# Optimization experiments

Hardware: AMD Instinct MI355X
Metric: run time of the kernel (lower is better)

## Reference

```python
import jax, jax.numpy as jnp
import numpy as np

B, S, D, H = 64, 65536, 512, 256
H2 = H // 2
CAP_LIMIT = 0.85
ACT_THR = 0.5


def _normalize(x):
    return x / jnp.maximum(jnp.linalg.norm(x, axis=-1, keepdims=True), 1e-12)


def _layernorm(x, g, b):
    m = x.mean(-1, keepdims=True)
    v = ((x - m) ** 2).mean(-1, keepdims=True)
    return (x - m) / jnp.sqrt(v + 1e-5) * g + b


def setup_inputs() -> dict:
    key = jax.random.key(0)
    ks = jax.random.split(key, 20)

    def lin(k, i, o):
        s = 1.0 / np.sqrt(i)
        kw, kb = jax.random.split(k)
        return (jax.random.uniform(kw, (i, o), minval=-s, maxval=s),
                jax.random.uniform(kb, (o,), minval=-s, maxval=s))

    inp = {}
    inp["new_content"] = jax.random.normal(ks[0], (B, D), dtype=jnp.float32)
    inp["query"] = jax.random.normal(ks[1], (B, D), dtype=jnp.float32)
    inp["memory_bank"] = jax.random.normal(ks[2], (S, D), dtype=jnp.float32)
    inp["access_times"] = jax.random.uniform(ks[3], (S,), minval=0.0, maxval=900.0)
    inp["current_step"] = 1000
    inp["sr_w1"], inp["sr_b1"] = lin(ks[4], 2 * D, H)
    inp["sr_g"] = jnp.ones((H,), jnp.float32)
    inp["sr_beta"] = jnp.zeros((H,), jnp.float32)
    inp["sr_w2"], inp["sr_b2"] = lin(ks[5], H, H2)
    inp["sn_w"], inp["sn_b"] = lin(ks[6], D, H2)
    inp["sg_w"], inp["sg_b"] = lin(ks[7], H2, 1)
    inp["el_w"], inp["el_b"] = lin(ks[8], 1, 32)
    inp["ec_w"], inp["ec_b"] = lin(ks[9], D, 32)
    inp["eg_w"], inp["eg_b"] = lin(ks[10], 64, 1)
    inp["dd_w1"], inp["dd_b1"] = lin(ks[11], 2 * D, H)
    inp["dd_w2"], inp["dd_b2"] = lin(ks[12], H, 1)
    inp["ds_w1"], inp["ds_b1"] = lin(ks[13], 2 * D, H)
    inp["ds_w2"], inp["ds_b2"] = lin(ks[14], H, 1)
    return inp


def _forward(new_content, query, memory_bank, access_times,
             sr_w1, sr_b1, sr_g, sr_beta, sr_w2, sr_b2,
             sn_w, sn_b, sg_w, sg_b,
             el_w, el_b, ec_w, ec_b, eg_w, eg_b,
             dd_w1, dd_b1, dd_w2, dd_b2,
             ds_w1, ds_b1, ds_w2, ds_b2,
             step):
    mem = memory_bank
    at = access_times
    norms = jnp.linalg.norm(mem, axis=-1)               # [S]
    capacity = jnp.mean((norms > ACT_THR).astype(jnp.float32))
    dyn_thr = jnp.clip(
        jnp.where(capacity < 0.3, 0.08,
                  jnp.where(capacity < 0.6, 0.08 + (capacity - 0.3) * 0.733,
                            0.3 + (capacity - 0.6))), 0.0, 0.7)
    topk_thr = jnp.where(capacity < 0.3, 0.1, jnp.where(capacity < 0.6, 0.2, 0.4))
    raw_thr = jnp.where(capacity < 0.3, 0.3, 0.5)

    # store relevance / novelty / gate
    combined = jnp.concatenate([new_content, query], -1)          # [B,2D]
    h = _layernorm(combined @ sr_w1 + sr_b1, sr_g, sr_beta)
    rel = jax.nn.relu(jax.nn.relu(h) @ sr_w2 + sr_b2)             # [B,H2]
    nn_ = _normalize(new_content)
    sims = nn_ @ _normalize(mem).T                                # [B,S]
    max_sim = sims.max(-1, keepdims=True)
    novelty = (1.0 - max_sim) / 2.0                               # [B,1]
    nf = jax.nn.sigmoid(new_content @ sn_w + sn_b)
    store_score = jax.nn.sigmoid((rel + nf) @ sg_w + sg_b)        # [B,1]

    # novelty percentile over active slots (no boolean-shape gather)
    active = norms > ACT_THR
    n_active = active.sum()
    nov_mean = novelty.mean()
    cond = (nov_mean > (1.0 - sims)) & active[None, :]
    denom = (new_content.shape[0] * jnp.maximum(n_active, 1)).astype(jnp.float32)
    perc = jnp.where(n_active > 0, cond.sum().astype(jnp.float32) / denom, 1.0)

    base_store = store_score.mean() > raw_thr
    novelty_ok = nov_mean > dyn_thr
    topk_ok = perc > topk_thr
    should_store = base_store & novelty_ok & topk_ok

    # emergency erase (capacity over limit)
    do_erase = capacity > CAP_LIMIT
    age = jnp.maximum(step - at, 0.0)
    es_em = age / (age.max() + 1e-6) + (1.0 - jax.nn.sigmoid(norms))
    victim = jnp.argmax(es_em)
    mem = jnp.where(do_erase, mem.at[victim].set(0.0), mem)
    at = jnp.where(do_erase, at.at[victim].set(-99999.0), at)
    should_store = should_store & jnp.logical_not(do_erase & jnp.logical_not(novelty_ok))

    # per-slot erase scores
    lru = jax.nn.relu(((step - at) / 1000.0)[:, None] @ el_w + el_b)   # [S,32]
    conf = jax.nn.sigmoid(mem @ ec_w + ec_b)                            # [S,32]
    erase_scores = jax.nn.sigmoid(jnp.concatenate([lru, conf], -1) @ eg_w + eg_b)[:, 0]

    # conflict detection: top-3 similar slots, gather-MLP-scatter drift
    sims2 = _normalize(new_content) @ _normalize(mem).T                # [B,S]
    tv, ti = jax.lax.top_k(sims2, 3)                                   # [B,3]
    cmask = (tv > 0.7) & (tv < 0.99)
    gathered = mem[ti]                                                 # [B,3,D]
    pair = jnp.concatenate([jnp.broadcast_to(new_content[:, None, :], gathered.shape), gathered], -1)
    prob = jax.nn.sigmoid(jax.nn.relu(pair @ dd_w1 + dd_b1) @ dd_w2 + dd_b2)[..., 0]
    strength = jax.nn.sigmoid(jax.nn.relu(pair @ ds_w1 + ds_b1) @ ds_w2 + ds_b2)[..., 0]
    apply_m = cmask & (prob > 0.5)                                     # [B,3]
    avg = (new_content[:, None, :] + gathered) / 2.0
    s = strength[..., None]
    dn_cand = (1.0 - s) * new_content[:, None, :] + s * avg
    do_cand = (1.0 - s) * gathered + s * avg
    drifted_new = new_content
    for k in range(3):  # fixed k=3, later k overwrites (matches torch inner loop)
        drifted_new = jnp.where(apply_m[:, k:k + 1], dn_cand[:, k], drifted_new)
    for k in range(3):
        idx = ti[:, k]
        cur = mem[idx]
        mem = mem.at[idx].set(jnp.where(apply_m[:, k, None], do_cand[:, k], cur))

    # conditional write
    slot_age = step - at
    recent = (at >= 0.0) & (slot_age < 3.0)
    masked = erase_scores * (~recent).astype(erase_scores.dtype)
    masked = jnp.where(masked.max() <= 0.0, slot_age, masked)
    write_idx = jnp.where(do_erase, victim, jnp.argmax(masked))
    erase_out = jnp.where(should_store & jnp.logical_not(do_erase), masked, erase_scores)
    mem = jnp.where(should_store, mem.at[write_idx].set(drifted_new[0]), mem)
    at = jnp.where(should_store, at.at[write_idx].set(step), at)

    recent_changes = jnp.abs(mem - memory_bank).mean()
    return (mem, at, erase_out, store_score[:, 0], novelty[:, 0], recent_changes)


def reference(new_content, query, memory_bank, access_times,
              sr_w1, sr_b1, sr_g, sr_beta, sr_w2, sr_b2,
              sn_w, sn_b, sg_w, sg_b,
              el_w, el_b, ec_w, ec_b, eg_w, eg_b,
              dd_w1, dd_b1, dd_w2, dd_b2,
              ds_w1, ds_b1, ds_w2, ds_b2,
              current_step):
    step = jnp.float32(current_step)
    return _forward(new_content, query, memory_bank, access_times,
                    sr_w1, sr_b1, sr_g, sr_beta, sr_w2, sr_b2,
                    sn_w, sn_b, sg_w, sg_b,
                    el_w, el_b, ec_w, ec_b, eg_w, eg_b,
                    dd_w1, dd_b1, dd_w2, dd_b2,
                    ds_w1, ds_b1, ds_w2, ds_b2, step)
```

## Files before the change

### kernel.cpp

```cpp
#include <hip/hip_runtime.h>
#include <math.h>
#include <limits.h>

#define S_N 65536
#define D_N 512
#define B_N 64

typedef __attribute__((ext_vector_type(8))) short short8;
typedef __attribute__((ext_vector_type(4))) float f32x4;

#define SIMS_F      (B_N*S_N/2)
#define OFF_SIMS    0
#define OFF_AEXT    (OFF_SIMS + SIMS_F)
#define AEXT_F      (96*512/2)
#define OFF_NORMS   (OFF_AEXT + AEXT_F)
#define OFF_CONF    (OFF_NORMS + S_N)
#define OFF_FLAGS   (OFF_CONF + S_N)
#define OFF_LIST    (OFF_FLAGS + S_N)
#define OFF_MASKED  (OFF_LIST + 256)
#define OFF_ERSC    (OFF_MASKED + S_N)
#define OFF_SLOTAGE (OFF_ERSC + S_N)
#define OFF_STORES  (OFF_SLOTAGE + S_N)
#define OFF_MAXSIM  (OFF_STORES + 64)
#define OFF_TI      (OFF_MAXSIM + 64)
#define OFF_TV      (OFF_TI + 192)
#define OFF_APPLY   (OFF_TV + 192)
#define OFF_HM      (OFF_APPLY + 192)
#define OFF_HNC     (OFF_HM + 32768)
#define OFF_HG      (OFF_HNC + 65536)
#define OFF_DNC0    (OFF_HG + 196608)
#define OFF_DRIFT0  (OFF_DNC0 + 1536)
#define OFF_DOCAND  (OFF_DRIFT0 + 512)
#define OFF_SCAL    (OFF_DOCAND + 98304)

#define OUT_MEM 0
#define OUT_AT  (S_N*D_N)
#define OUT_ER  (OUT_AT + S_N)
#define OUT_SS  (OUT_ER + S_N)
#define OUT_NOV (OUT_SS + 64)
#define OUT_RC  (OUT_NOV + 64)

struct __align__(8) Scal {
  unsigned long long victim_pack;
  unsigned long long masked_pack;
  unsigned long long slotage_pack;
  int cnt_active;
  int cond_cnt;
  unsigned age_max_t;
  float nov_mean;
  float changed_sum;
  int do_erase;
  int should_store;
  int write_idx;
  int victim_idx;
  int list_cnt;
};

__device__ __forceinline__ float sigmoidf_(float x){ return 1.0f/(1.0f+expf(-x)); }
__device__ __forceinline__ unsigned f2mono(float f){
  unsigned u = __float_as_uint(f);
  return (u & 0x80000000u) ? ~u : (u | 0x80000000u);
}
__device__ __forceinline__ float mono2f(unsigned m){
  unsigned u = (m & 0x80000000u) ? (m & 0x7FFFFFFFu) : ~m;
  return __uint_as_float(u);
}
__device__ __forceinline__ unsigned long long packvi(float v, int i){
  return (((unsigned long long)f2mono(v)) << 32) | (unsigned long long)(0xFFFFFFFFu - (unsigned)i);
}
__device__ __forceinline__ bool betterVI(float v, int i, float v2, int i2){
  return (v > v2) || (v == v2 && i < i2);
}
__device__ __forceinline__ unsigned short bf16r(float f){
  unsigned u = __float_as_uint(f);
  return (unsigned short)((u + 0x7fffu + ((u>>16)&1u)) >> 16);
}
__device__ __forceinline__ float bf2f(unsigned short h){
  return __uint_as_float(((unsigned)h)<<16);
}
__device__ __forceinline__ void touch_row(int row, float* ws){
  int* flags = (int*)(ws + OFF_FLAGS);
  if (atomicExch(&flags[row], 1) == 0){
    Scal* sc = (Scal*)(ws + OFF_SCAL);
    int i = atomicAdd(&sc->list_cnt, 1);
    ((int*)(ws + OFF_LIST))[i] = row;
  }
}

__global__ __launch_bounds__(256) void k_init(const float* __restrict__ nc,
                                              const float* __restrict__ at_in,
                                              const float* __restrict__ ec_w,
                                              const int* __restrict__ step_p,
                                              float* __restrict__ ws, float* __restrict__ out){
  int blk = blockIdx.x, t = threadIdx.x;
  Scal* sc = (Scal*)(ws + OFF_SCAL);
  unsigned short* aB = (unsigned short*)(ws + OFF_AEXT);
  if (blk == 0){
    if (t == 0){
      sc->victim_pack = 0ULL; sc->masked_pack = 0ULL; sc->slotage_pack = 0ULL;
      sc->cnt_active = 0; sc->cond_cnt = 0; sc->age_max_t = 0u;
      sc->nov_mean = 0.0f; sc->changed_sum = 0.0f;
      sc->do_erase = 0; sc->should_store = 0; sc->write_idx = 0; sc->victim_idx = 0;
      sc->list_cnt = 0;
    }
    if (t < 64) ((unsigned*)(ws + OFF_MAXSIM))[t] = 0u;
  } else if (blk <= 64){
    int b = blk - 1;
    __shared__ float red[256];
    float x0 = nc[b*512 + t], x1 = nc[b*512 + 256 + t];
    red[t] = x0*x0 + x1*x1;
    __syncthreads();
    for (int o=128;o>0;o>>=1){ if (t<o) red[t]+=red[t+o]; __syncthreads(); }
    float inv = 1.0f / fmaxf(sqrtf(red[0]), 1e-12f);
    aB[b*512 + t]       = bf16r(x0*inv);
    aB[b*512 + 256 + t] = bf16r(x1*inv);
  } else if (blk <= 96){
    int j = blk - 65;
    for (int d=t; d<512; d+=256) aB[(64+j)*512 + d] = bf16r(ec_w[d*32 + j]);
  } else if (blk <= 160){
    int part = blk - 97;
    float stepf = (float)step_p[0];
    float lmax = -1e30f;
    for (int s = part*1024 + t; s < (part+1)*1024; s += 256)
      lmax = fmaxf(lmax, fmaxf(stepf - at_in[s], 0.0f));
    __shared__ float red[256];
    red[t]=lmax; __syncthreads();
    for (int o=128;o>0;o>>=1){ if (t<o) red[t]=fmaxf(red[t],red[t+o]); __syncthreads(); }
    if (t==0) atomicMax(&sc->age_max_t, f2mono(red[0]));
  } else if (blk <= 224){
    int part = blk - 161;
    for (int s = part*1024 + t; s < (part+1)*1024; s += 256)
      out[OUT_AT + s] = at_in[s];
  } else {
    int part = blk - 225;
    int* flags = (int*)(ws + OFF_FLAGS);
    for (int s = part*1024 + t; s < (part+1)*1024; s += 256) flags[s] = 0;
  }
}

#define BT_ST 520
__global__ __launch_bounds__(256,2) void k_phase1(const float* __restrict__ mem,
                                                  const float* __restrict__ ec_b,
                                                  const float* __restrict__ eg_w,
                                                  float* __restrict__ ws, float* __restrict__ out){
  __shared__ unsigned short lB[64*BT_ST];
  __shared__ float nred[256];
  __shared__ float linv[64];
  __shared__ unsigned lmax[64];
  int t = threadIdx.x;
  int s0 = blockIdx.x * 64;
  if (t < 64) lmax[t] = 0u;
  Scal* sc = (Scal*)(ws + OFF_SCAL);

  const float4* mem4 = (const float4*)(mem + (size_t)s0*512);
  float4* out4 = (float4*)(out + OUT_MEM + (size_t)s0*512);
  #pragma unroll
  for (int i=0;i<32;i++){
    int idx = i*256 + t;
    float4 v = mem4[idx];
    out4[idx] = v;
    int row = idx >> 7, c4 = idx & 127;
    unsigned u0 = (((unsigned)bf16r(v.y))<<16) | bf16r(v.x);
    unsigned u1 = (((unsigned)bf16r(v.w))<<16) | bf16r(v.z);
    uint2* dst = (uint2*)&lB[row*BT_ST + c4*4];
    *dst = make_uint2(u0,u1);
  }
  __syncthreads();

  {
    int row = t>>2, q = t&3;
    const unsigned* src = (const unsigned*)&lB[row*BT_ST + q*128];
    float ssq = 0.f;
    #pragma unroll
    for (int i=0;i<64;i++){
      unsigned u = src[i];
      float a = __uint_as_float(u<<16);
      float b = __uint_as_float(u & 0xffff0000u);
      ssq = fmaf(a,a,ssq); ssq = fmaf(b,b,ssq);
    }
    nred[t] = ssq;
  }
  __syncthreads();
  if (t < 64){
    float s2 = nred[t*4]+nred[t*4+1]+nred[t*4+2]+nred[t*4+3];
    float nrm = sqrtf(s2);
    ws[OFF_NORMS + s0 + t] = nrm;
    linv[t] = 1.0f / fmaxf(nrm, 1e-12f);
    unsigned long long m = __ballot(nrm > 0.5f);
    if (t == 0) atomicAdd(&sc->cnt_active, (int)__popcll(m));
  }
  __syncthreads();

  int lane = t & 63, wv = t >> 6;
  int quad = lane >> 4, l15 = lane & 15;
  const unsigned short* aB = (const unsigned short*)(ws + OFF_AEXT);
  f32x4 acc[6];
  #pragma unroll
  for (int r=0;r<6;r++) acc[r] = (f32x4){0.f,0.f,0.f,0.f};
  #pragma unroll 4
  for (int kc=0;kc<16;kc++){
    int kb = kc*32 + quad*8;
    short8 bfrag = *(const short8*)&lB[(wv*16 + l15)*BT_ST + kb];
    #pragma unroll
    for (int rt=0;rt<6;rt++){
      short8 afrag = *(const short8*)&aB[(rt*16 + l15)*512 + kb];
      acc[rt] = __builtin_amdgcn_mfma_f32_16x16x32_bf16(afrag, bfrag, acc[rt], 0,0,0);
    }
  }

  float lv = linv[wv*16 + l15];
  unsigned short* simsb = (unsigned short*)(ws + OFF_SIMS);
  #pragma unroll
  for (int rt=0;rt<4;rt++){
    #pragma unroll
    for (int r=0;r<4;r++){
      int a = rt*16 + quad*4 + r;
      float sim = acc[rt][r] * lv;
      simsb[(size_t)a*S_N + s0 + wv*16 + l15] = bf16r(sim);
      atomicMax(&lmax[a], f2mono(sim));
    }
  }
  float cpart = 0.f;
  #pragma unroll
  for (int rt=4;rt<6;rt++){
    #pragma unroll
    for (int r=0;r<4;r++){
      int j = (rt-4)*16 + quad*4 + r;
      cpart += sigmoidf_(acc[rt][r] + ec_b[j]) * eg_w[32+j];
    }
  }
  cpart += __shfl_down(cpart, 32);
  cpart += __shfl_down(cpart, 16);
  if (l15 < 16 && quad == 0) ws[OFF_CONF + s0 + wv*16 + l15] = cpart;
  __syncthreads();
  if (t < 64) atomicMax(((unsigned*)(ws + OFF_MAXSIM)) + t, lmax[t]);
}

__global__ __launch_bounds__(256) void k_mlp1a(const float* __restrict__ nc, const float* __restrict__ qr,
    const float* __restrict__ sr_w1, float* __restrict__ ws){
  int blk = blockIdx.x, t = threadIdx.x;
  int b = blk >> 1, half = blk & 1;
  __shared__ float ch[512];
  const float* src = half ? qr : nc;
  ch[t] = src[b*512 + t]; ch[256+t] = src[b*512 + 256 + t];
  __syncthreads();
  float h = 0.f;
  const float* w = sr_w1 + (half*512)*256 + t;
  for (int i=0;i<512;i++) h = fmaf(ch[i], w[i*256], h);
  ws[OFF_HM + (half*64 + b)*256 + t] = h;
}

__global__ __launch_bounds__(256) void k_mlp1b(const float* __restrict__ nc, const float* __restrict__ qr,
    const float* __restrict__ sr_b1, const float* __restrict__ sr_g, const float* __restrict__ sr_beta,
    const float* __restrict__ sr_w2, const float* __restrict__ sr_b2,
    const float* __restrict__ sn_w,  const float* __restrict__ sn_b,
    const float* __restrict__ sg_w,  const float* __restrict__ sg_b,
    float* __restrict__ ws, float* __restrict__ out){
  int b = blockIdx.x, t = threadIdx.x;
  Scal* sc = (Scal*)(ws + OFF_SCAL);
  __shared__ float red[256];
  if (b == 64){
    const unsigned* gms = (const unsigned*)(ws + OFF_MAXSIM);
    float nv = 0.0f;
    if (t < 64){
      float msim = mono2f(gms[t]);
      nv = (1.0f - msim) * 0.5f;
      out[OUT_NOV + t] = nv;
    }
    red[t] = (t < 64) ? nv : 0.0f;
    __syncthreads();
    for (int o=128;o>0;o>>=1){ if (t<o) red[t]+=red[t+o]; __syncthreads(); }
    if (t == 0) sc->nov_mean = red[0] / 64.0f;
    return;
  }
  __shared__ float comb[1024];
  __shared__ float hbuf[256];
  comb[t]       = nc[b*512 + t];
  comb[256 + t] = nc[b*512 + 256 + t];
  comb[512 + t] = qr[b*512 + t];
  comb[768 + t] = qr[b*512 + 256 + t];
  float h = ws[OFF_HM + b*256 + t] + ws[OFF_HM + (64 + b)*256 + t] + sr_b1[t];
  red[t] = h; __syncthreads();
  for (int o=128;o>0;o>>=1){ if (t<o) red[t]+=red[t+o]; __syncthreads(); }
  float mean = red[0] / 256.0f;
  __syncthreads();
  float dx = h - mean;
  red[t] = dx*dx; __syncthreads();
  for (int o=128;o>0;o>>=1){ if (t<o) red[t]+=red[t+o]; __syncthreads(); }
  float var = red[0] / 256.0f;
  __syncthreads();
  float hn = dx / sqrtf(var + 1e-5f) * sr_g[t] + sr_beta[t];
  hbuf[t] = fmaxf(hn, 0.0f);
  __syncthreads();
  float val = 0.0f;
  if (t < 128){
    float r = sr_b2[t];
    for (int j=0;j<256;j++) r = fmaf(hbuf[j], sr_w2[j*128 + t], r);
    r = fmaxf(r, 0.0f);
    float nf = sn_b[t];
    for (int d=0; d<512; d++) nf = fmaf(comb[d], sn_w[d*128 + t], nf);
    nf = sigmoidf_(nf);
    val = (r + nf) * sg_w[t];
  }
  red[t] = val; __syncthreads();
  for (int o=128;o>0;o>>=1){ if (t<o) red[t]+=red[t+o]; __syncthreads(); }
  if (t == 0){
    float ssc = sigmoidf_(red[0] + sg_b[0]);
    out[OUT_SS + b] = ssc;
    ws[OFF_STORES + b] = ssc;
  }
}

__global__ __launch_bounds__(256) void k_scan(const float* __restrict__ at_in,
                                              const int* __restrict__ step_p,
                                              float* __restrict__ ws){
  int t = threadIdx.x;
  Scal* sc = (Scal*)(ws + OFF_SCAL);
  float thr = 1.0f - sc->nov_mean;
  float stepf = (float)step_p[0];
  float agemax = mono2f(sc->age_max_t);
  const unsigned* simsu = (const unsigned*)(ws + OFF_SIMS);
  const float* norms = ws + OFF_NORMS;
  int gid = blockIdx.x*256 + t;
  int gstride = gridDim.x*256;
  int cnt = 0;
  for (int idx = gid; idx < B_N*S_N/2; idx += gstride){
    unsigned u = simsu[idx];
    int s = (idx*2) & (S_N-1);
    float v0 = __uint_as_float(u<<16);
    float v1 = __uint_as_float(u & 0xffff0000u);
    if (v0 > thr && norms[s]   > 0.5f) cnt++;
    if (v1 > thr && norms[s+1] > 0.5f) cnt++;
  }
  unsigned long long best = 0ULL;
  for (int s = gid; s < S_N; s += gstride){
    float age = fmaxf(stepf - at_in[s], 0.0f);
    float es = age/(agemax + 1e-6f) + (1.0f - sigmoidf_(norms[s]));
    unsigned long long pk = packvi(es, s);
    if (pk > best) best = pk;
  }
  __shared__ int redc[256];
  __shared__ unsigned long long redp[256];
  redc[t] = cnt; redp[t] = best;
  __syncthreads();
  for (int o=128;o>0;o>>=1){
    if (t<o){ redc[t]+=redc[t+o]; if (redp[t+o] > redp[t]) redp[t]=redp[t+o]; }
    __syncthreads();
  }
  if (t == 0){
    atomicAdd(&sc->cond_cnt, redc[0]);
    atomicMax(&sc->victim_pack, redp[0]);
  }
}

__global__ __launch_bounds__(256) void k_victimfix(const float* __restrict__ ec_b,
                                                   const float* __restrict__ eg_w,
                                                   float* __restrict__ ws, float* __restrict__ out){
  int t = threadIdx.x;
  Scal* sc = (Scal*)(ws + OFF_SCAL);
  float capacity = (float)sc->cnt_active / 65536.0f;
  int de = (capacity > 0.85f) ? 1 : 0;
  int victim = (int)(0xFFFFFFFFu - (unsigned)(sc->victim_pack & 0xFFFFFFFFULL));
  if (t == 0){ sc->do_erase = de; sc->victim_idx = victim; }
  if (de){
    for (int d=t; d<512; d+=256) out[OUT_MEM + victim*512 + d] = 0.0f;
    if (t == 0){
      out[OUT_AT + victim] = -99999.0f;
      touch_row(victim, ws);
      float sum = 0.0f;
      for (int j=0;j<32;j++) sum += sigmoidf_(ec_b[j]) * eg_w[32 + j];
      ws[OFF_CONF + victim] = sum;
    }
  }
}

__global__ __launch_bounds__(256) void k_top3(float* __restrict__ ws){
  int b = blockIdx.x, t = threadIdx.x;
  Scal* sc = (Scal*)(ws + OFF_SCAL);
  int de = sc->do_erase;
  int victim = sc->victim_idx;
  const unsigned short* simrow = (const unsigned short*)(ws + OFF_SIMS) + (size_t)b*S_N;
  float v[3] = {-1e30f,-1e30f,-1e30f};
  int ix[3] = {INT_MAX, INT_MAX, INT_MAX};
  for (int s = t; s < S_N; s += 256){
    float val = bf2f(simrow[s]);
    if (de && s == victim) val = 0.0f;
    if (betterVI(val, s, v[2], ix[2])){
      if (betterVI(val, s, v[1], ix[1])){
        if (betterVI(val, s, v[0], ix[0])){
          v[2]=v[1]; ix[2]=ix[1]; v[1]=v[0]; ix[1]=ix[0]; v[0]=val; ix[0]=s;
        } else { v[2]=v[1]; ix[2]=ix[1]; v[1]=val; ix[1]=s; }
      } else { v[2]=val; ix[2]=s; }
    }
  }
  __shared__ float sv[256*3];
  __shared__ int   si[256*3];
  for (int r=0;r<3;r++){ sv[t*3+r]=v[r]; si[t*3+r]=ix[r]; }
  for (int off=128; off>0; off>>=1){
    __syncthreads();
    if (t < off){
      float av[3], bv[3], ov[3]; int ai[3], bi[3], oi[3];
      for (int r=0;r<3;r++){ av[r]=sv[t*3+r]; ai[r]=si[t*3+r]; bv[r]=sv[(t+off)*3+r]; bi[r]=si[(t+off)*3+r]; }
      int ap=0, bp=0;
      for (int r=0;r<3;r++){
        bool takeA = (bp>=3) || (ap<3 && betterVI(av[ap],ai[ap],bv[bp],bi[bp]));
        if (takeA){ ov[r]=av[ap]; oi[r]=ai[ap]; ap++; }
        else      { ov[r]=bv[bp]; oi[r]=bi[bp]; bp++; }
      }
      for (int r=0;r<3;r++){ sv[t*3+r]=ov[r]; si[t*3+r]=oi[r]; }
    }
  }
  __syncthreads();
  if (t == 0){
    for (int k=0;k<3;k++){
      ws[OFF_TV + b*3 + k] = sv[k];
      ((int*)(ws + OFF_TI))[b*3 + k] = si[k];
    }
  }
}

__global__ __launch_bounds__(256) void k_mlp2(const float* __restrict__ nc,
    const float* __restrict__ dd_w1, const float* __restrict__ ds_w1,
    float* __restrict__ ws, float* __restrict__ out){
  int blk = blockIdx.x, t = threadIdx.x;
  int b = blk >> 2, ks = blk & 3;
  __shared__ float ch[3*256];
  if (ks < 2){
    ch[t] = nc[b*512 + ks*256 + t];
    __syncthreads();
    float hd = 0.f, hs = 0.f;
    const float* wd = dd_w1 + (ks*256)*256 + t;
    const float* wq = ds_w1 + (ks*256)*256 + t;
    for (int i=0;i<256;i++){
      float c = ch[i];
      hd = fmaf(c, wd[i*256], hd);
      hs = fmaf(c, wq[i*256], hs);
    }
    float* H = ws + OFF_HNC + ((ks*64 + b)*2)*256;
    H[t] = hd; H[256 + t] = hs;
  } else {
    int ks2 = ks - 2;
    const int* tip = (const int*)(ws + OFF_TI);
    int r0 = tip[b*3], r1 = tip[b*3+1], r2 = tip[b*3+2];
    ch[t]       = out[OUT_MEM + (size_t)r0*512 + ks2*256 + t];
    ch[256 + t] = out[OUT_MEM + (size_t)r1*512 + ks2*256 + t];
    ch[512 + t] = out[OUT_MEM + (size_t)r2*512 + ks2*256 + t];
    __syncthreads();
    float hd0=0,hd1=0,hd2=0,hs0=0,hs1=0,hs2=0;
    const float* wd = dd_w1 + (512 + ks2*256)*256 + t;
    const float* wq = ds_w1 + (512 + ks2*256)*256 + t;
    for (int i=0;i<256;i++){
      float w0 = wd[i*256], w1 = wq[i*256];
      float c0 = ch[i], c1 = ch[256+i], c2 = ch[512+i];
      hd0=fmaf(c0,w0,hd0); hd1=fmaf(c1,w0,hd1); hd2=fmaf(c2,w0,hd2);
      hs0=fmaf(c0,w1,hs0); hs1=fmaf(c1,w1,hs1); hs2=fmaf(c2,w1,hs2);
    }
    float* H = ws + OFF_HG;
    int p0 = b*3;
    H[((ks2*192 + p0+0)*2+0)*256 + t] = hd0;
    H[((ks2*192 + p0+1)*2+0)*256 + t] = hd1;
    H[((ks2*192 + p0+2)*2+0)*256 + t] = hd2;
    H[((ks2*192 + p0+0)*2+1)*256 + t] = hs0;
    H[((ks2*192 + p0+1)*2+1)*256 + t] = hs1;
    H[((ks2*192 + p0+2)*2+1)*256 + t] = hs2;
  }
}

__global__ __launch_bounds__(256) void k_pairfin(const float* __restrict__ nc,
    const float* __restrict__ dd_b1, const float* __restrict__ dd_w2, const float* __restrict__ dd_b2,
    const float* __restrict__ ds_b1, const float* __restrict__ ds_w2, const float* __restrict__ ds_b2,
    float* __restrict__ ws, float* __restrict__ out){
  int p = blockIdx.x, t = threadIdx.x;
  int b = p / 3, k = p - 3*b;
  const int* tip = (const int*)(ws + OFF_TI);
  int row = tip[p];
  float hd = ws[OFF_HNC + ((0*64+b)*2+0)*256 + t] + ws[OFF_HNC + ((1*64+b)*2+0)*256 + t]
           + ws[OFF_HG + ((0*192+p)*2+0)*256 + t] + ws[OFF_HG + ((1*192+p)*2+0)*256 + t] + dd_b1[t];
  float hs = ws[OFF_HNC + ((0*64+b)*2+1)*256 + t] + ws[OFF_HNC + ((1*64+b)*2+1)*256 + t]
           + ws[OFF_HG + ((0*192+p)*2+1)*256 + t] + ws[OFF_HG + ((1*192+p)*2+1)*256 + t] + ds_b1[t];
  __shared__ float red[256];
  __shared__ float bc[2];
  red[t] = fmaxf(hd, 0.f) * dd_w2[t];
  __syncthreads();
  for (int o=128;o>0;o>>=1){ if (t<o) red[t]+=red[t+o]; __syncthreads(); }
  if (t == 0) bc[0] = red[0] + dd_b2[0];
  __syncthreads();
  red[t] = fmaxf(hs, 0.f) * ds_w2[t];
  __syncthreads();
  for (int o=128;o>0;o>>=1){ if (t<o) red[t]+=red[t+o]; __syncthreads(); }
  if (t == 0) bc[1] = red[0] + ds_b2[0];
  __syncthreads();
  float prob  = sigmoidf_(bc[0]);
  float stren = sigmoidf_(bc[1]);
  float tvv = ws[OFF_TV + p];
  int ap = (tvv > 0.7f && tvv < 0.99f && prob > 0.5f) ? 1 : 0;
  if (t == 0){
    ((int*)(ws + OFF_APPLY))[p] = ap;
    touch_row(row, ws);
  }
  for (int d=t; d<512; d+=256){
    float n = nc[b*512 + d];
    float g = out[OUT_MEM + (size_t)row*512 + d];
    float avg = 0.5f*(n + g);
    ws[OFF_DOCAND + p*512 + d] = (1.0f - stren)*g + stren*avg;
    if (b == 0) ws[OFF_DNC0 + k*512 + d] = (1.0f - stren)*n + stren*avg;
  }
}

__global__ __launch_bounds__(64) void k_scatter(float* __restrict__ ws, float* __restrict__ out){
  int d = blockIdx.x*64 + threadIdx.x;
  const int* tip = (const int*)(ws + OFF_TI);
  const int* ap  = (const int*)(ws + OFF_APPLY);
  for (int k=0;k<3;k++){
    float cur[64];
    #pragma unroll
    for (int b=0;b<64;b++) cur[b] = out[OUT_MEM + (size_t)tip[b*3 + k]*512 + d];
    #pragma unroll
    for (int b=0;b<64;b++){
      int p = b*3 + k;
      float v = ap[p] ? ws[OFF_DOCAND + p*512 + d] : cur[b];
      out[OUT_MEM + (size_t)tip[p]*512 + d] = v;
    }
  }
}

__global__ __launch_bounds__(256) void k_erase(const int* __restrict__ step_p,
    const float* __restrict__ el_w, const float* __restrict__ el_b,
    const float* __restrict__ eg_w, const float* __restrict__ eg_b,
    float* __restrict__ ws, float* __restrict__ out){
  int t = threadIdx.x;
  Scal* sc = (Scal*)(ws + OFF_SCAL);
  float stepf = (float)step_p[0];
  float egb = eg_b[0];
  int gid = blockIdx.x*256 + t;
  int gstride = gridDim.x*256;
  unsigned long long bm = 0ULL, bs = 0ULL;
  for (int s = gid; s < S_N; s += gstride){
    float a = out[OUT_AT + s];
    float x = (stepf - a) / 1000.0f;
    float lp = 0.0f;
    #pragma unroll
    for (int j=0;j<32;j++) lp += fmaxf(x*el_w[j] + el_b[j], 0.0f) * eg_w[j];
    float er = sigmoidf_(lp + ws[OFF_CONF + s] + egb);
    float sa = stepf - a;
    bool recent = (a >= 0.0f) && (sa < 3.0f);
    float msk = recent ? 0.0f : er;
    ws[OFF_ERSC + s] = er;
    ws[OFF_MASKED + s] = msk;
    ws[OFF_SLOTAGE + s] = sa;
    unsigned long long pm = packvi(msk, s); if (pm > bm) bm = pm;
    unsigned long long ps = packvi(sa,  s); if (ps > bs) bs = ps;
  }
  __shared__ unsigned long long rm[256], rs[256];
  rm[t]=bm; rs[t]=bs; __syncthreads();
  for (int o=128;o>0;o>>=1){
    if (t<o){ if (rm[t+o]>rm[t]) rm[t]=rm[t+o]; if (rs[t+o]>rs[t]) rs[t]=rs[t+o]; }
    __syncthreads();
  }
  if (t == 0){
    atomicMax(&sc->masked_pack, rm[0]);
    atomicMax(&sc->slotage_pack, rs[0]);
  }
}

__global__ __launch_bounds__(64) void k_decide(const float* __restrict__ nc, float* __restrict__ ws){
  int t = threadIdx.x;
  Scal* sc = (Scal*)(ws + OFF_SCAL);
  __shared__ float red[64];
  red[t] = ws[OFF_STORES + t];
  __syncthreads();
  for (int o=32;o>0;o>>=1){ if (t<o) red[t]+=red[t+o]; __syncthreads(); }
  if (t == 0){
    float store_mean = red[0] / 64.0f;
    int cnt = sc->cnt_active;
    float capacity = (float)cnt / 65536.0f;
    float dyn_thr;
    if (capacity < 0.3f) dyn_thr = 0.08f;
    else if (capacity < 0.6f) dyn_thr = 0.08f + (capacity - 0.3f)*0.733f;
    else dyn_thr = 0.3f + (capacity - 0.6f);
    dyn_thr = fminf(fmaxf(dyn_thr, 0.0f), 0.7f);
    float topk_thr = (capacity < 0.3f) ? 0.1f : ((capacity < 0.6f) ? 0.2f : 0.4f);
    float raw_thr  = (capacity < 0.3f) ? 0.3f : 0.5f;
    int base_store = store_mean > raw_thr;
    int novelty_ok = sc->nov_mean > dyn_thr;
    int cmax = cnt > 1 ? cnt : 1;
    float denom = (float)(64 * cmax);
    float perc = (cnt > 0) ? ((float)sc->cond_cnt) / denom : 1.0f;
    int topk_ok = perc > topk_thr;
    int de = sc->do_erase;
    int ss = base_store && novelty_ok && topk_ok;
    if (de && !novelty_ok) ss = 0;
    float mmax = mono2f((unsigned)(sc->masked_pack >> 32));
    int marg = (int)(0xFFFFFFFFu - (unsigned)(sc->masked_pack  & 0xFFFFFFFFULL));
    int sarg = (int)(0xFFFFFFFFu - (unsigned)(sc->slotage_pack & 0xFFFFFFFFULL));
    sc->should_store = ss;
    sc->write_idx = de ? sc->victim_idx : ((mmax > 0.0f) ? marg : sarg);
  }
  __syncthreads();
  const int* ap = (const int*)(ws + OFF_APPLY);
  for (int d=t; d<512; d+=64){
    float v = nc[d];
    if (ap[0]) v = ws[OFF_DNC0 + 0*512 + d];
    if (ap[1]) v = ws[OFF_DNC0 + 1*512 + d];
    if (ap[2]) v = ws[OFF_DNC0 + 2*512 + d];
    ws[OFF_DRIFT0 + d] = v;
  }
}

__global__ __launch_bounds__(256) void k_finalout(const int* __restrict__ step_p,
                                                  float* __restrict__ ws, float* __restrict__ out){
  int blk = blockIdx.x, t = threadIdx.x;
  Scal* sc = (Scal*)(ws + OFF_SCAL);
  int ss = sc->should_store, de = sc->do_erase;
  if (blk == 64){
    if (ss){
      int wi = sc->write_idx;
      for (int d=t; d<512; d+=256) out[OUT_MEM + (size_t)wi*512 + d] = ws[OFF_DRIFT0 + d];
      if (t == 0){
        out[OUT_AT + wi] = (float)step_p[0];
        touch_row(wi, ws);
      }
    }
    return;
  }
  float mmax = mono2f((unsigned)(sc->masked_pack >> 32));
  bool usemask = ss && !de;
  for (int s = blk*256 + t; s < S_N; s += 64*256){
    float v;
    if (usemask) v = (mmax <= 0.0f) ? ws[OFF_SLOTAGE + s] : ws[OFF_MASKED + s];
    else v = ws[OFF_ERSC + s];
    out[OUT_ER + s] = v;
  }
}

__global__ __launch_bounds__(256) void k_diff(const float* __restrict__ mem,
                                              float* __restrict__ ws, float* __restrict__ out){
  int t = threadIdx.x;
  Scal* sc = (Scal*)(ws + OFF_SCAL);
  int cnt = sc->list_cnt;
  const int* list = (const int*)(ws + OFF_LIST);
  float lsum = 0.0f;
  for (int i = blockIdx.x; i < cnt; i += gridDim.x){
    int row = list[i];
    float part = 0.0f;
    for (int d=t; d<512; d+=256)
      part += fabsf(out[OUT_MEM + (size_t)row*512 + d] - mem[(size_t)row*512 + d]);
    lsum += part;
  }
  __shared__ float red[256];
  red[t] = lsum; __syncthreads();
  for (int o=128;o>0;o>>=1){ if (t<o) red[t]+=red[t+o]; __syncthreads(); }
  if (t == 0 && red[0] != 0.0f) atomicAdd(&sc->changed_sum, red[0]);
}

__global__ void k_rc(float* __restrict__ ws, float* __restrict__ out){
  if (threadIdx.x == 0 && blockIdx.x == 0){
    Scal* sc = (Scal*)(ws + OFF_SCAL);
    out[OUT_RC] = sc->changed_sum / 33554432.0f;
  }
}

extern "C" void kernel_launch(void* const* d_in, const int* in_sizes, int n_in,
                              void* d_out, int out_size, void* d_ws, size_t ws_size,
                              hipStream_t stream) {
  const float* nc    = (const float*)d_in[0];
  const float* qr    = (const float*)d_in[1];
  const float* mem   = (const float*)d_in[2];
  const float* at    = (const float*)d_in[3];
  const int*   step  = (const int*)  d_in[4];
  const float* sr_w1 = (const float*)d_in[5];
  const float* sr_b1 = (const float*)d_in[6];
  const float* sr_g  = (const float*)d_in[7];
  const float* sr_be = (const float*)d_in[8];
  const float* sr_w2 = (const float*)d_in[9];
  const float* sr_b2 = (const float*)d_in[10];
  const float* sn_w  = (const float*)d_in[11];
  const float* sn_b  = (const float*)d_in[12];
  const float* sg_w  = (const float*)d_in[13];
  const float* sg_b  = (const float*)d_in[14];
  const float* el_w  = (const float*)d_in[15];
  const float* el_b  = (const float*)d_in[16];
  const float* ec_w  = (const float*)d_in[17];
  const float* ec_b  = (const float*)d_in[18];
  const float* eg_w  = (const float*)d_in[19];
  const float* eg_b  = (const float*)d_in[20];
  const float* dd_w1 = (const float*)d_in[21];
  const float* dd_b1 = (const float*)d_in[22];
  const float* dd_w2 = (const float*)d_in[23];
  const float* dd_b2 = (const float*)d_in[24];
  const float* ds_w1 = (const float*)d_in[25];
  const float* ds_b1 = (const float*)d_in[26];
  const float* ds_w2 = (const float*)d_in[27];
  const float* ds_b2 = (const float*)d_in[28];
  float* out = (float*)d_out;
  float* ws  = (float*)d_ws;

  k_init     <<<dim3(289), dim3(256), 0, stream>>>(nc, at, ec_w, step, ws, out);
  k_mlp1a    <<<dim3(128), dim3(256), 0, stream>>>(nc, qr, sr_w1, ws);
  k_phase1   <<<dim3(1024), dim3(256), 0, stream>>>(mem, ec_b, eg_w, ws, out);
  k_mlp1b    <<<dim3(65), dim3(256), 0, stream>>>(nc, qr, sr_b1, sr_g, sr_be,
                                                  sr_w2, sr_b2, sn_w, sn_b, sg_w, sg_b, ws, out);
  k_scan     <<<dim3(512), dim3(256), 0, stream>>>(at, step, ws);
  k_victimfix<<<dim3(1), dim3(256), 0, stream>>>(ec_b, eg_w, ws, out);
  k_top3     <<<dim3(64), dim3(256), 0, stream>>>(ws);
  k_mlp2     <<<dim3(256), dim3(256), 0, stream>>>(nc, dd_w1, ds_w1, ws, out);
  k_pairfin  <<<dim3(192), dim3(256), 0, stream>>>(nc, dd_b1, dd_w2, dd_b2,
                                                   ds_b1, ds_w2, ds_b2, ws, out);
  k_scatter  <<<dim3(8), dim3(64), 0, stream>>>(ws, out);
  k_erase    <<<dim3(64), dim3(256), 0, stream>>>(step, el_w, el_b, eg_w, eg_b, ws, out);
  k_decide   <<<dim3(1), dim3(64), 0, stream>>>(nc, ws);
  k_finalout <<<dim3(65), dim3(256), 0, stream>>>(step, ws, out);
  k_diff     <<<dim3(64), dim3(256), 0, stream>>>(mem, ws, out);
  k_rc       <<<dim3(1), dim3(64), 0, stream>>>(ws, out);
}
```

Baseline: 583.9 us.

## Fuse kernel pipeline and stream memory rows directly into MFMA fragments

After: 645.9 us. 10.6% more time.

```diff
diff --git a/kernel.cpp b/kernel.cpp
--- a/kernel.cpp
+++ b/kernel.cpp
@@ -25,13 +25,14 @@
 #define OFF_TI      (OFF_MAXSIM + 64)
 #define OFF_TV      (OFF_TI + 192)
 #define OFF_APPLY   (OFF_TV + 192)
-#define OFF_HM      (OFF_APPLY + 192)
-#define OFF_HNC     (OFF_HM + 32768)
-#define OFF_HG      (OFF_HNC + 65536)
-#define OFF_DNC0    (OFF_HG + 196608)
+#define OFF_WIN     (OFF_APPLY + 192)
+#define OFF_T4      (OFF_WIN + 192)
+#define OFF_DNC0    (OFF_T4 + 2048)
 #define OFF_DRIFT0  (OFF_DNC0 + 1536)
 #define OFF_DOCAND  (OFF_DRIFT0 + 512)
-#define OFF_SCAL    (OFF_DOCAND + 98304)
+#define OFF_HNC     (OFF_DOCAND + 98304)
+#define OFF_HG      (OFF_HNC + 65536)
+#define OFF_SCAL    (OFF_HG + 196608)
 
 #define OUT_MEM 0
 #define OUT_AT  (S_N*D_N)
@@ -54,6 +55,7 @@
   int write_idx;
   int victim_idx;
   int list_cnt;
+  int done;
 };
 
 __device__ __forceinline__ float sigmoidf_(float x){ return 1.0f/(1.0f+expf(-x)); }
@@ -71,9 +73,9 @@
 __device__ __forceinline__ bool betterVI(float v, int i, float v2, int i2){
   return (v > v2) || (v == v2 && i < i2);
 }
-__device__ __forceinline__ unsigned short bf16r(float f){
+__device__ __forceinline__ unsigned bf16r(float f){
   unsigned u = __float_as_uint(f);
-  return (unsigned short)((u + 0x7fffu + ((u>>16)&1u)) >> 16);
+  return (u + 0x7fffu + ((u>>16)&1u)) >> 16;
 }
 __device__ __forceinline__ float bf2f(unsigned short h){
   return __uint_as_float(((unsigned)h)<<16);
@@ -86,12 +88,30 @@
     ((int*)(ws + OFF_LIST))[i] = row;
   }
 }
+__device__ __forceinline__ void victim_vals(float stepf,
+    const float* el_w, const float* el_b, const float* eg_w, const float* eg_b,
+    const float* ec_b, float* er_v, float* slot_v, float* conf0){
+  float x = (stepf + 99999.0f) / 1000.0f;
+  float lp = 0.0f, c0 = 0.0f;
+  #pragma unroll
+  for (int j=0;j<32;j++){
+    lp += fmaxf(x*el_w[j] + el_b[j], 0.0f) * eg_w[j];
+    c0 += sigmoidf_(ec_b[j]) * eg_w[32 + j];
+  }
+  *conf0 = c0;
+  *er_v = sigmoidf_(lp + c0 + eg_b[0]);
+  *slot_v = stepf + 99999.0f;
+}
 
 __global__ __launch_bounds__(256) void k_init(const float* __restrict__ nc,
-                                              const float* __restrict__ at_in,
-                                              const float* __restrict__ ec_w,
-                                              const int* __restrict__ step_p,
-                                              float* __restrict__ ws, float* __restrict__ out){
+    const float* __restrict__ qr, const float* __restrict__ at_in,
+    const float* __restrict__ ec_w, const int* __restrict__ step_p,
+    const float* __restrict__ sr_w1, const float* __restrict__ sr_b1,
+    const float* __restrict__ sr_g,  const float* __restrict__ sr_beta,
+    const float* __restrict__ sr_w2, const float* __restrict__ sr_b2,
+    const float* __restrict__ sn_w,  const float* __restrict__ sn_b,
+    const float* __restrict__ sg_w,  const float* __restrict__ sg_b,
+    float* __restrict__ ws, float* __restrict__ out){
   int blk = blockIdx.x, t = threadIdx.x;
   Scal* sc = (Scal*)(ws + OFF_SCAL);
   unsigned short* aB = (unsigned short*)(ws + OFF_AEXT);
@@ -101,7 +121,7 @@
       sc->cnt_active = 0; sc->cond_cnt = 0; sc->age_max_t = 0u;
       sc->nov_mean = 0.0f; sc->changed_sum = 0.0f;
       sc->do_erase = 0; sc->should_store = 0; sc->write_idx = 0; sc->victim_idx = 0;
-      sc->list_cnt = 0;
+      sc->list_cnt = 0; sc->done = 0;
     }
     if (t < 64) ((unsigned*)(ws + OFF_MAXSIM))[t] = 0u;
   } else if (blk <= 64){
@@ -112,11 +132,11 @@
     __syncthreads();
     for (int o=128;o>0;o>>=1){ if (t<o) red[t]+=red[t+o]; __syncthreads(); }
     float inv = 1.0f / fmaxf(sqrtf(red[0]), 1e-12f);
-    aB[b*512 + t]       = bf16r(x0*inv);
-    aB[b*512 + 256 + t] = bf16r(x1*inv);
+    aB[b*512 + t]       = (unsigned short)bf16r(x0*inv);
+    aB[b*512 + 256 + t] = (unsigned short)bf16r(x1*inv);
   } else if (blk <= 96){
     int j = blk - 65;
-    for (int d=t; d<512; d+=256) aB[(64+j)*512 + d] = bf16r(ec_w[d*32 + j]);
+    for (int d=t; d<512; d+=256) aB[(64+j)*512 + d] = (unsigned short)bf16r(ec_w[d*32 + j]);
   } else if (blk <= 160){
     int part = blk - 97;
     float stepf = (float)step_p[0];
@@ -131,93 +151,135 @@
     int part = blk - 161;
     for (int s = part*1024 + t; s < (part+1)*1024; s += 256)
       out[OUT_AT + s] = at_in[s];
-  } else {
+  } else if (blk <= 288){
     int part = blk - 225;
     int* flags = (int*)(ws + OFF_FLAGS);
     for (int s = part*1024 + t; s < (part+1)*1024; s += 256) flags[s] = 0;
-  }
-}
-
-#define BT_ST 520
-__global__ __launch_bounds__(256,2) void k_phase1(const float* __restrict__ mem,
-                                                  const float* __restrict__ ec_b,
-                                                  const float* __restrict__ eg_w,
-                                                  float* __restrict__ ws, float* __restrict__ out){
-  __shared__ unsigned short lB[64*BT_ST];
-  __shared__ float nred[256];
-  __shared__ float linv[64];
-  __shared__ unsigned lmax[64];
+  } else {
+    int b = blk - 289;
+    __shared__ float comb[1024];
+    __shared__ float hbuf[256];
+    __shared__ float red[256];
+    comb[t]       = nc[b*512 + t];
+    comb[256 + t] = nc[b*512 + 256 + t];
+    comb[512 + t] = qr[b*512 + t];
+    comb[768 + t] = qr[b*512 + 256 + t];
+    __syncthreads();
+    float h0=0.f,h1=0.f,h2=0.f,h3=0.f;
+    const float* w = sr_w1 + t;
+    for (int i=0;i<1024;i+=4){
+      h0 = fmaf(comb[i],   w[(i  )*256], h0);
+      h1 = fmaf(comb[i+1], w[(i+1)*256], h1);
+      h2 = fmaf(comb[i+2], w[(i+2)*256], h2);
+      h3 = fmaf(comb[i+3], w[(i+3)*256], h3);
+    }
+    float h = ((h0+h1)+(h2+h3)) + sr_b1[t];
+    red[t] = h; __syncthreads();
+    for (int o=128;o>0;o>>=1){ if (t<o) red[t]+=red[t+o]; __syncthreads(); }
+    float mean = red[0] / 256.0f;
+    __syncthreads();
+    float dx = h - mean;
+    red[t] = dx*dx; __syncthreads();
+    for (int o=128;o>0;o>>=1){ if (t<o) red[t]+=red[t+o]; __syncthreads(); }
+    float var = red[0] / 256.0f;
+    __syncthreads();
+    float hn = dx / sqrtf(var + 1e-5f) * sr_g[t] + sr_beta[t];
+    hbuf[t] = fmaxf(hn, 0.0f);
+    __syncthreads();
+    float val = 0.0f;
+    if (t < 128){
+      float r0=0.f, r1=0.f;
+      const float* w2 = sr_w2 + t;
+      for (int j=0;j<256;j+=2){
+        r0 = fmaf(hbuf[j],   w2[(j  )*128], r0);
+        r1 = fmaf(hbuf[j+1], w2[(j+1)*128], r1);
+      }
+      float r = fmaxf(r0+r1+sr_b2[t], 0.0f);
+      float n0=0.f,n1=0.f,n2=0.f,n3=0.f;
+      const float* wn = sn_w + t;
+      for (int d=0; d<512; d+=4){
+        n0 = fmaf(comb[d],   wn[(d  )*128], n0);
+        n1 = fmaf(comb[d+1], wn[(d+1)*128], n1);
+        n2 = fmaf(comb[d+2], wn[(d+2)*128], n2);
+        n3 = fmaf(comb[d+3], wn[(d+3)*128], n3);
+      }
+      float nf = sigmoidf_(((n0+n1)+(n2+n3)) + sn_b[t]);
+      val = (r + nf) * sg_w[t];
+    }
+    red[t] = val; __syncthreads();
+    for (int o=128;o>0;o>>=1){ if (t<o) red[t]+=red[t+o]; __syncthreads(); }
+    if (t == 0){
+      float ssc = sigmoidf_(red[0] + sg_b[0]);
+      out[OUT_SS + b] = ssc;
+      ws[OFF_STORES + b] = ssc;
+    }
+  }
+}
+
+__global__ __launch_bounds__(256,4) void k_phase1(const float* __restrict__ mem,
+    const float* __restrict__ ec_b, const float* __restrict__ eg_w,
+    float* __restrict__ ws, float* __restrict__ out){
   int t = threadIdx.x;
   int s0 = blockIdx.x * 64;
-  if (t < 64) lmax[t] = 0u;
-  Scal* sc = (Scal*)(ws + OFF_SCAL);
-
-  const float4* mem4 = (const float4*)(mem + (size_t)s0*512);
-  float4* out4 = (float4*)(out + OUT_MEM + (size_t)s0*512);
-  #pragma unroll
-  for (int i=0;i<32;i++){
-    int idx = i*256 + t;
-    float4 v = mem4[idx];
-    out4[idx] = v;
-    int row = idx >> 7, c4 = idx & 127;
-    unsigned u0 = (((unsigned)bf16r(v.y))<<16) | bf16r(v.x);
-    unsigned u1 = (((unsigned)bf16r(v.w))<<16) | bf16r(v.z);
-    uint2* dst = (uint2*)&lB[row*BT_ST + c4*4];
-    *dst = make_uint2(u0,u1);
-  }
-  __syncthreads();
-
-  {
-    int row = t>>2, q = t&3;
-    const unsigned* src = (const unsigned*)&lB[row*BT_ST + q*128];
-    float ssq = 0.f;
-    #pragma unroll
-    for (int i=0;i<64;i++){
-      unsigned u = src[i];
-      float a = __uint_as_float(u<<16);
-      float b = __uint_as_float(u & 0xffff0000u);
-      ssq = fmaf(a,a,ssq); ssq = fmaf(b,b,ssq);
-    }
-    nred[t] = ssq;
-  }
-  __syncthreads();
-  if (t < 64){
-    float s2 = nred[t*4]+nred[t*4+1]+nred[t*4+2]+nred[t*4+3];
-    float nrm = sqrtf(s2);
-    ws[OFF_NORMS + s0 + t] = nrm;
-    linv[t] = 1.0f / fmaxf(nrm, 1e-12f);
-    unsigned long long m = __ballot(nrm > 0.5f);
-    if (t == 0) atomicAdd(&sc->cnt_active, (int)__popcll(m));
-  }
-  __syncthreads();
-
   int lane = t & 63, wv = t >> 6;
   int quad = lane >> 4, l15 = lane & 15;
+  int row = wv*16 + l15;
+  const float* rp = mem + (size_t)(s0 + row)*512 + quad*8;
+  float*       op = out + OUT_MEM + (size_t)(s0 + row)*512 + quad*8;
   const unsigned short* aB = (const unsigned short*)(ws + OFF_AEXT);
+  Scal* sc = (Scal*)(ws + OFF_SCAL);
   f32x4 acc[6];
   #pragma unroll
   for (int r=0;r<6;r++) acc[r] = (f32x4){0.f,0.f,0.f,0.f};
+  float ssq = 0.f;
   #pragma unroll 4
   for (int kc=0;kc<16;kc++){
+    float4 a0 = *(const float4*)(rp + kc*32);
+    float4 a1 = *(const float4*)(rp + kc*32 + 4);
+    *(float4*)(op + kc*32)     = a0;
+    *(float4*)(op + kc*32 + 4) = a1;
+    ssq = fmaf(a0.x,a0.x,ssq); ssq = fmaf(a0.y,a0.y,ssq);
+    ssq = fmaf(a0.z,a0.z,ssq); ssq = fmaf(a0.w,a0.w,ssq);
+    ssq = fmaf(a1.x,a1.x,ssq); ssq = fmaf(a1.y,a1.y,ssq);
+    ssq = fmaf(a1.z,a1.z,ssq); ssq = fmaf(a1.w,a1.w,ssq);
+    union { short8 s8; unsigned u[4]; } bf;
+    bf.u[0] = (bf16r(a0.y)<<16) | bf16r(a0.x);
+    bf.u[1] = (bf16r(a0.w)<<16) | bf16r(a0.z);
+    bf.u[2] = (bf16r(a1.y)<<16) | bf16r(a1.x);
+    bf.u[3] = (bf16r(a1.w)<<16) | bf16r(a1.z);
     int kb = kc*32 + quad*8;
-    short8 bfrag = *(const short8*)&lB[(wv*16 + l15)*BT_ST + kb];
     #pragma unroll
     for (int rt=0;rt<6;rt++){
-      short8 afrag = *(const short8*)&aB[(rt*16 + l15)*512 + kb];
-      acc[rt] = __builtin_amdgcn_mfma_f32_16x16x32_bf16(afrag, bfrag, acc[rt], 0,0,0);
-    }
-  }
-
-  float lv = linv[wv*16 + l15];
+      short8 af = *(const short8*)&aB[(rt*16 + l15)*512 + kb];
+      acc[rt] = __builtin_amdgcn_mfma_f32_16x16x32_bf16(af, bf.s8, acc[rt], 0,0,0);
+    }
+  }
+  ssq += __shfl_xor(ssq, 16);
+  ssq += __shfl_xor(ssq, 32);
+  float nrm = sqrtf(ssq);
+  float inv = 1.0f / fmaxf(nrm, 1e-12f);
+  if (quad == 0) ws[OFF_NORMS + s0 + row] = nrm;
+  __shared__ int cnt4[4];
+  unsigned long long bal = __ballot(quad==0 && nrm > 0.5f);
+  if (lane == 0) cnt4[wv] = (int)__popcll(bal);
   unsigned short* simsb = (unsigned short*)(ws + OFF_SIMS);
+  unsigned* gmsu = (unsigned*)(ws + OFF_MAXSIM);
   #pragma unroll
   for (int rt=0;rt<4;rt++){
     #pragma unroll
     for (int r=0;r<4;r++){
       int a = rt*16 + quad*4 + r;
-      float sim = acc[rt][r] * lv;
-      simsb[(size_t)a*S_N + s0 + wv*16 + l15] = bf16r(sim);
-      atomicMax(&lmax[a], f2mono(sim));
+      float sim = acc[rt][r] * inv;
+      simsb[(size_t)a*S_N + s0 + row] = (unsigned short)bf16r(sim);
+      float m = sim;
+      m = fmaxf(m, __shfl_xor(m, 1));
+      m = fmaxf(m, __shfl_xor(m, 2));
+      m = fmaxf(m, __shfl_xor(m, 4));
+      m = fmaxf(m, __shfl_xor(m, 8));
+      if (l15 == 0){
+        unsigned mm = f2mono(m);
+        if (mm > gmsu[a]) atomicMax(&gmsu[a], mm);
+      }
     }
   }
   float cpart = 0.f;
@@ -229,192 +291,205 @@
       cpart += sigmoidf_(acc[rt][r] + ec_b[j]) * eg_w[32+j];
     }
   }
-  cpart += __shfl_down(cpart, 32);
-  cpart += __shfl_down(cpart, 16);
-  if (l15 < 16 && quad == 0) ws[OFF_CONF + s0 + wv*16 + l15] = cpart;
-  __syncthreads();
-  if (t < 64) atomicMax(((unsigned*)(ws + OFF_MAXSIM)) + t, lmax[t]);
-}
-
-__global__ __launch_bounds__(256) void k_mlp1a(const float* __restrict__ nc, const float* __restrict__ qr,
-    const float* __restrict__ sr_w1, float* __restrict__ ws){
+  cpart += __shfl_xor(cpart, 16);
+  cpart += __shfl_xor(cpart, 32);
+  if (quad == 0) ws[OFF_CONF + s0 + row] = cpart;
+  __syncthreads();
+  if (t == 0) atomicAdd(&sc->cnt_active, cnt4[0]+cnt4[1]+cnt4[2]+cnt4[3]);
+}
+
+__global__ __launch_bounds__(256) void k_scan(const float* __restrict__ at_in,
+    const int* __restrict__ step_p,
+    const float* __restrict__ el_w, const float* __restrict__ el_b,
+    const float* __restrict__ eg_w, const float* __restrict__ eg_b,
+    float* __restrict__ ws, float* __restrict__ out){
   int blk = blockIdx.x, t = threadIdx.x;
-  int b = blk >> 1, half = blk & 1;
-  __shared__ float ch[512];
-  const float* src = half ? qr : nc;
-  ch[t] = src[b*512 + t]; ch[256+t] = src[b*512 + 256 + t];
-  __syncthreads();
-  float h = 0.f;
-  const float* w = sr_w1 + (half*512)*256 + t;
-  for (int i=0;i<512;i++) h = fmaf(ch[i], w[i*256], h);
-  ws[OFF_HM + (half*64 + b)*256 + t] = h;
-}
-
-__global__ __launch_bounds__(256) void k_mlp1b(const float* __restrict__ nc, const float* __restrict__ qr,
-    const float* __restrict__ sr_b1, const float* __restrict__ sr_g, const float* __restrict__ sr_beta,
-    const float* __restrict__ sr_w2, const float* __restrict__ sr_b2,
-    const float* __restrict__ sn_w,  const float* __restrict__ sn_b,
-    const float* __restrict__ sg_w,  const float* __restrict__ sg_b,
+  Scal* sc = (Scal*)(ws + OFF_SCAL);
+  float stepf = (float)step_p[0];
+  if (blk < 512){
+    __shared__ float nred[64];
+    const unsigned* gms = (const unsigned*)(ws + OFF_MAXSIM);
+    if (t < 64){
+      float nv = (1.0f - mono2f(gms[t])) * 0.5f;
+      nred[t] = nv;
+      if (blk == 0) out[OUT_NOV + t] = nv;
+    }
+    __syncthreads();
+    if (t < 32) nred[t] += nred[t+32];
+    __syncthreads();
+    if (t < 16) nred[t] += nred[t+16];
+    __syncthreads();
+    if (t < 8)  nred[t] += nred[t+8];
+    __syncthreads();
+    if (t < 4)  nred[t] += nred[t+4];
+    __syncthreads();
+    float nov_mean = (nred[0]+nred[1]+nred[2]+nred[3]) / 64.0f;
+    if (blk == 0 && t == 0) sc->nov_mean = nov_mean;
+    float thr = 1.0f - nov_mean;
+    float agemax = mono2f(sc->age_max_t);
+    const unsigned* simsu = (const unsigned*)(ws + OFF_SIMS);
+    const float* norms = ws + OFF_NORMS;
+    int gid = blk*256 + t;
+    int gstride = 512*256;
+    int cnt = 0;
+    for (int idx = gid; idx < B_N*S_N/2; idx += gstride){
+      unsigned u = simsu[idx];
+      int s = (idx*2) & (S_N-1);
+      float v0 = __uint_as_float(u<<16);
+      float v1 = __uint_as_float(u & 0xffff0000u);
+      if (v0 > thr && norms[s]   > 0.5f) cnt++;
+      if (v1 > thr && norms[s+1] > 0.5f) cnt++;
+    }
+    unsigned long long best = 0ULL;
+    for (int s = gid; s < S_N; s += gstride){
+      float age = fmaxf(stepf - at_in[s], 0.0f);
+      float es = age/(agemax + 1e-6f) + (1.0f - sigmoidf_(norms[s]));
+      unsigned long long pk = packvi(es, s);
+      if (pk > best) best = pk;
+    }
+    __shared__ int redc[256];
+    __shared__ unsigned long long redp[256];
+    redc[t] = cnt; redp[t] = best;
+    __syncthreads();
+    for (int o=128;o>0;o>>=1){
+      if (t<o){ redc[t]+=redc[t+o]; if (redp[t+o] > redp[t]) redp[t]=redp[t+o]; }
+      __syncthreads();
+    }
+    if (t == 0){
+      atomicAdd(&sc->cond_cnt, redc[0]);
+      atomicMax(&sc->victim_pack, redp[0]);
+    }
+  } else if (blk < 768){
+    int idx = blk - 512;
+    int b = idx >> 2, ch = idx & 3;
+    const unsigned short* simrow = (const unsigned short*)(ws + OFF_SIMS) + (size_t)b*S_N + ch*16384;
+    float v[4] = {-1e30f,-1e30f,-1e30f,-1e30f};
+    int ix[4] = {INT_MAX,INT_MAX,INT_MAX,INT_MAX};
+    for (int s = t; s < 16384; s += 256){
+      int gs = ch*16384 + s;
+      float val = bf2f(simrow[s]);
+      if (betterVI(val, gs, v[3], ix[3])){
+        if (betterVI(val, gs, v[1], ix[1])){
+          if (betterVI(val, gs, v[0], ix[0])){
+            v[3]=v[2];ix[3]=ix[2]; v[2]=v[1];ix[2]=ix[1]; v[1]=v[0];ix[1]=ix[0]; v[0]=val;ix[0]=gs;
+          } else { v[3]=v[2];ix[3]=ix[2]; v[2]=v[1];ix[2]=ix[1]; v[1]=val;ix[1]=gs; }
+        } else {
+          if (betterVI(val, gs, v[2], ix[2])){ v[3]=v[2];ix[3]=ix[2]; v[2]=val;ix[2]=gs; }
+          else { v[3]=val; ix[3]=gs; }
+        }
+      }
+    }
+    __shared__ float sv[256*4];
+    __shared__ int   si[256*4];
+    for (int r=0;r<4;r++){ sv[t*4+r]=v[r]; si[t*4+r]=ix[r]; }
+    for (int off=128; off>0; off>>=1){
+      __syncthreads();
+      if (t < off){
+        float av[4], bv[4], ov[4]; int ai[4], bi[4], oi[4];
+        for (int r=0;r<4;r++){ av[r]=sv[t*4+r]; ai[r]=si[t*4+r]; bv[r]=sv[(t+off)*4+r]; bi[r]=si[(t+off)*4+r]; }
+        int ap=0, bp=0;
+        for (int r=0;r<4;r++){
+          bool takeA = (bp>=4) || (ap<4 && betterVI(av[ap],ai[ap],bv[bp],bi[bp]));
+          if (takeA){ ov[r]=av[ap]; oi[r]=ai[ap]; ap++; }
+          else      { ov[r]=bv[bp]; oi[r]=bi[bp]; bp++; }
+        }
+        for (int r=0;r<4;r++){ sv[t*4+r]=ov[r]; si[t*4+r]=oi[r]; }
+      }
+    }
+    __syncthreads();
+    if (t == 0){
+      for (int r=0;r<4;r++){
+        ws[OFF_T4 + idx*8 + r] = sv[r];
+        ((int*)ws)[OFF_T4 + idx*8 + 4 + r] = si[r];
+      }
+    }
+  } else {
+    int q = blk - 768;
+    float egb = eg_b[0];
+    for (int s = q*1024 + t; s < (q+1)*1024; s += 256){
+      float a = at_in[s];
+      float x = (stepf - a) / 1000.0f;
+      float lp = 0.0f;
+      #pragma unroll
+      for (int j=0;j<32;j++) lp += fmaxf(x*el_w[j] + el_b[j], 0.0f) * eg_w[j];
+      float er = sigmoidf_(lp + ws[OFF_CONF + s] + egb);
+      float sa = stepf - a;
+      bool recent = (a >= 0.0f) && (sa < 3.0f);
+      ws[OFF_ERSC + s] = er;
+      ws[OFF_MASKED + s] = recent ? 0.0f : er;
+      ws[OFF_SLOTAGE + s] = sa;
+    }
+  }
+}
+
+__global__ __launch_bounds__(256) void k_victop(const int* __restrict__ step_p,
+    const float* __restrict__ el_w, const float* __restrict__ el_b,
+    const float* __restrict__ eg_w, const float* __restrict__ eg_b,
+    const float* __restrict__ ec_b,
     float* __restrict__ ws, float* __restrict__ out){
-  int b = blockIdx.x, t = threadIdx.x;
+  int blk = blockIdx.x, t = threadIdx.x;
   Scal* sc = (Scal*)(ws + OFF_SCAL);
-  __shared__ float red[256];
-  if (b == 64){
-    const unsigned* gms = (const unsigned*)(ws + OFF_MAXSIM);
-    float nv = 0.0f;
-    if (t < 64){
-      float msim = mono2f(gms[t]);
-      nv = (1.0f - msim) * 0.5f;
-      out[OUT_NOV + t] = nv;
-    }
-    red[t] = (t < 64) ? nv : 0.0f;
-    __syncthreads();
-    for (int o=128;o>0;o>>=1){ if (t<o) red[t]+=red[t+o]; __syncthreads(); }
-    if (t == 0) sc->nov_mean = red[0] / 64.0f;
-    return;
-  }
-  __shared__ float comb[1024];
-  __shared__ float hbuf[256];
-  comb[t]       = nc[b*512 + t];
-  comb[256 + t] = nc[b*512 + 256 + t];
-  comb[512 + t] = qr[b*512 + t];
-  comb[768 + t] = qr[b*512 + 256 + t];
-  float h = ws[OFF_HM + b*256 + t] + ws[OFF_HM + (64 + b)*256 + t] + sr_b1[t];
-  red[t] = h; __syncthreads();
-  for (int o=128;o>0;o>>=1){ if (t<o) red[t]+=red[t+o]; __syncthreads(); }
-  float mean = red[0] / 256.0f;
-  __syncthreads();
-  float dx = h - mean;
-  red[t] = dx*dx; __syncthreads();
-  for (int o=128;o>0;o>>=1){ if (t<o) red[t]+=red[t+o]; __syncthreads(); }
-  float var = red[0] / 256.0f;
-  __syncthreads();
-  float hn = dx / sqrtf(var + 1e-5f) * sr_g[t] + sr_beta[t];
-  hbuf[t] = fmaxf(hn, 0.0f);
-  __syncthreads();
-  float val = 0.0f;
-  if (t < 128){
-    float r = sr_b2[t];
-    for (int j=0;j<256;j++) r = fmaf(hbuf[j], sr_w2[j*128 + t], r);
-    r = fmaxf(r, 0.0f);
-    float nf = sn_b[t];
-    for (int d=0; d<512; d++) nf = fmaf(comb[d], sn_w[d*128 + t], nf);
-    nf = sigmoidf_(nf);
-    val = (r + nf) * sg_w[t];
-  }
-  red[t] = val; __syncthreads();
-  for (int o=128;o>0;o>>=1){ if (t<o) red[t]+=red[t+o]; __syncthreads(); }
-  if (t == 0){
-    float ssc = sigmoidf_(red[0] + sg_b[0]);
-    out[OUT_SS + b] = ssc;
-    ws[OFF_STORES + b] = ssc;
-  }
-}
-
-__global__ __launch_bounds__(256) void k_scan(const float* __restrict__ at_in,
-                                              const int* __restrict__ step_p,
-                                              float* __restrict__ ws){
-  int t = threadIdx.x;
-  Scal* sc = (Scal*)(ws + OFF_SCAL);
-  float thr = 1.0f - sc->nov_mean;
   float stepf = (float)step_p[0];
-  float agemax = mono2f(sc->age_max_t);
-  const unsigned* simsu = (const unsigned*)(ws + OFF_SIMS);
-  const float* norms = ws + OFF_NORMS;
-  int gid = blockIdx.x*256 + t;
-  int gstride = gridDim.x*256;
-  int cnt = 0;
-  for (int idx = gid; idx < B_N*S_N/2; idx += gstride){
-    unsigned u = simsu[idx];
-    int s = (idx*2) & (S_N-1);
-    float v0 = __uint_as_float(u<<16);
-    float v1 = __uint_as_float(u & 0xffff0000u);
-    if (v0 > thr && norms[s]   > 0.5f) cnt++;
-    if (v1 > thr && norms[s+1] > 0.5f) cnt++;
-  }
-  unsigned long long best = 0ULL;
-  for (int s = gid; s < S_N; s += gstride){
-    float age = fmaxf(stepf - at_in[s], 0.0f);
-    float es = age/(agemax + 1e-6f) + (1.0f - sigmoidf_(norms[s]));
-    unsigned long long pk = packvi(es, s);
-    if (pk > best) best = pk;
-  }
-  __shared__ int redc[256];
-  __shared__ unsigned long long redp[256];
-  redc[t] = cnt; redp[t] = best;
-  __syncthreads();
-  for (int o=128;o>0;o>>=1){
-    if (t<o){ redc[t]+=redc[t+o]; if (redp[t+o] > redp[t]) redp[t]=redp[t+o]; }
-    __syncthreads();
-  }
-  if (t == 0){
-    atomicAdd(&sc->cond_cnt, redc[0]);
-    atomicMax(&sc->victim_pack, redp[0]);
-  }
-}
-
-__global__ __launch_bounds__(256) void k_victimfix(const float* __restrict__ ec_b,
-                                                   const float* __restrict__ eg_w,
-                                                   float* __restrict__ ws, float* __restrict__ out){
-  int t = threadIdx.x;
-  Scal* sc = (Scal*)(ws + OFF_SCAL);
-  float capacity = (float)sc->cnt_active / 65536.0f;
-  int de = (capacity > 0.85f) ? 1 : 0;
+  int de = ((float)sc->cnt_active / 65536.0f > 0.85f) ? 1 : 0;
   int victim = (int)(0xFFFFFFFFu - (unsigned)(sc->victim_pack & 0xFFFFFFFFULL));
-  if (t == 0){ sc->do_erase = de; sc->victim_idx = victim; }
-  if (de){
-    for (int d=t; d<512; d+=256) out[OUT_MEM + victim*512 + d] = 0.0f;
+  if (blk == 0){
+    if (t == 0){ sc->do_erase = de; sc->victim_idx = victim; }
+    if (de){
+      for (int d=t; d<512; d+=256) out[OUT_MEM + (size_t)victim*512 + d] = 0.0f;
+      if (t == 0){
+        float er_v, slot_v, c0;
+        victim_vals(stepf, el_w, el_b, eg_w, eg_b, ec_b, &er_v, &slot_v, &c0);
+        out[OUT_AT + victim] = -99999.0f;
+        ws[OFF_CONF + victim] = c0;
+        ws[OFF_ERSC + victim] = er_v;
+        ws[OFF_MASKED + victim] = er_v;
+        ws[OFF_SLOTAGE + victim] = slot_v;
+        touch_row(victim, ws);
+      }
+    }
+  } else if (blk <= 64){
     if (t == 0){
-      out[OUT_AT + victim] = -99999.0f;
-      touch_row(victim, ws);
-      float sum = 0.0f;
-      for (int j=0;j<32;j++) sum += sigmoidf_(ec_b[j]) * eg_w[32 + j];
-      ws[OFF_CONF + victim] = sum;
-    }
-  }
-}
-
-__global__ __launch_bounds__(256) void k_top3(float* __restrict__ ws){
-  int b = blockIdx.x, t = threadIdx.x;
-  Scal* sc = (Scal*)(ws + OFF_SCAL);
-  int de = sc->do_erase;
-  int victim = sc->victim_idx;
-  const unsigned short* simrow = (const unsigned short*)(ws + OFF_SIMS) + (size_t)b*S_N;
-  float v[3] = {-1e30f,-1e30f,-1e30f};
-  int ix[3] = {INT_MAX, INT_MAX, INT_MAX};
-  for (int s = t; s < S_N; s += 256){
-    float val = bf2f(simrow[s]);
-    if (de && s == victim) val = 0.0f;
-    if (betterVI(val, s, v[2], ix[2])){
-      if (betterVI(val, s, v[1], ix[1])){
-        if (betterVI(val, s, v[0], ix[0])){
-          v[2]=v[1]; ix[2]=ix[1]; v[1]=v[0]; ix[1]=ix[0]; v[0]=val; ix[0]=s;
-        } else { v[2]=v[1]; ix[2]=ix[1]; v[1]=val; ix[1]=s; }
-      } else { v[2]=val; ix[2]=s; }
-    }
-  }
-  __shared__ float sv[256*3];
-  __shared__ int   si[256*3];
-  for (int r=0;r<3;r++){ sv[t*3+r]=v[r]; si[t*3+r]=ix[r]; }
-  for (int off=128; off>0; off>>=1){
-    __syncthreads();
-    if (t < off){
-      float av[3], bv[3], ov[3]; int ai[3], bi[3], oi[3];
-      for (int r=0;r<3;r++){ av[r]=sv[t*3+r]; ai[r]=si[t*3+r]; bv[r]=sv[(t+off)*3+r]; bi[r]=si[(t+off)*3+r]; }
-      int ap=0, bp=0;
-      for (int r=0;r<3;r++){
-        bool takeA = (bp>=3) || (ap<3 && betterVI(av[ap],ai[ap],bv[bp],bi[bp]));
-        if (takeA){ ov[r]=av[ap]; oi[r]=ai[ap]; ap++; }
-        else      { ov[r]=bv[bp]; oi[r]=bi[bp]; bp++; }
-      }
-      for (int r=0;r<3;r++){ sv[t*3+r]=ov[r]; si[t*3+r]=oi[r]; }
-    }
-  }
-  __syncthreads();
-  if (t == 0){
-    for (int k=0;k<3;k++){
-      ws[OFF_TV + b*3 + k] = sv[k];
-      ((int*)(ws + OFF_TI))[b*3 + k] = si[k];
+      int b = blk - 1;
+      float cv[17]; int ci[17]; int n = 0;
+      for (int ch=0; ch<4; ch++){
+        int idx = b*4 + ch;
+        for (int r=0;r<4;r++){
+          float v = ws[OFF_T4 + idx*8 + r];
+          int ii = ((const int*)ws)[OFF_T4 + idx*8 + 4 + r];
+          if (de && ii == victim) continue;
+          cv[n] = v; ci[n] = ii; n++;
+        }
+      }
+      if (de){ cv[n] = 0.0f; ci[n] = victim; n++; }
+      for (int k=0;k<3;k++){
+        int bi = 0;
+        for (int j=1;j<n;j++) if (betterVI(cv[j],ci[j],cv[bi],ci[bi])) bi = j;
+        ws[OFF_TV + b*3 + k] = cv[bi];
+        ((int*)(ws + OFF_TI))[b*3 + k] = ci[bi];
+        cv[bi] = -1e30f; ci[bi] = INT_MAX;
+      }
+    }
+  } else {
+    int q = blk - 65;
+    float er_v = 0.f, slot_v = 0.f, c0;
+    if (de) victim_vals(stepf, el_w, el_b, eg_w, eg_b, ec_b, &er_v, &slot_v, &c0);
+    unsigned long long bm = 0ULL, bs = 0ULL;
+    for (int s = q*1024 + t; s < (q+1)*1024; s += 256){
+      float msk = ws[OFF_MASKED + s];
+      float sa  = ws[OFF_SLOTAGE + s];
+      if (de && s == victim){ msk = er_v; sa = slot_v; }
+      unsigned long long pm = packvi(msk, s); if (pm > bm) bm = pm;
+      unsigned long long ps = packvi(sa,  s); if (ps > bs) bs = ps;
+    }
+    __shared__ unsigned long long rm[256], rs[256];
+    rm[t]=bm; rs[t]=bs; __syncthreads();
+    for (int o=128;o>0;o>>=1){
+      if (t<o){ if (rm[t+o]>rm[t]) rm[t]=rm[t+o]; if (rs[t+o]>rs[t]) rs[t]=rs[t+o]; }
+      __syncthreads();
+    }
+    if (t == 0){
+      atomicMax(&sc->masked_pack, rm[0]);
+      atomicMax(&sc->slotage_pack, rs[0]);
     }
   }
 }
@@ -494,10 +569,7 @@
   float stren = sigmoidf_(bc[1]);
   float tvv = ws[OFF_TV + p];
   int ap = (tvv > 0.7f && tvv < 0.99f && prob > 0.5f) ? 1 : 0;
-  if (t == 0){
-    ((int*)(ws + OFF_APPLY))[p] = ap;
-    touch_row(row, ws);
-  }
+  if (t == 0) ((int*)(ws + OFF_APPLY))[p] = ap;
   for (int d=t; d<512; d+=256){
     float n = nc[b*512 + d];
     float g = out[OUT_MEM + (size_t)row*512 + d];
@@ -507,71 +579,22 @@
   }
 }
 
-__global__ __launch_bounds__(64) void k_scatter(float* __restrict__ ws, float* __restrict__ out){
-  int d = blockIdx.x*64 + threadIdx.x;
-  const int* tip = (const int*)(ws + OFF_TI);
-  const int* ap  = (const int*)(ws + OFF_APPLY);
-  for (int k=0;k<3;k++){
-    float cur[64];
-    #pragma unroll
-    for (int b=0;b<64;b++) cur[b] = out[OUT_MEM + (size_t)tip[b*3 + k]*512 + d];
-    #pragma unroll
-    for (int b=0;b<64;b++){
-      int p = b*3 + k;
-      float v = ap[p] ? ws[OFF_DOCAND + p*512 + d] : cur[b];
-      out[OUT_MEM + (size_t)tip[p]*512 + d] = v;
-    }
-  }
-}
-
-__global__ __launch_bounds__(256) void k_erase(const int* __restrict__ step_p,
-    const float* __restrict__ el_w, const float* __restrict__ el_b,
-    const float* __restrict__ eg_w, const float* __restrict__ eg_b,
-    float* __restrict__ ws, float* __restrict__ out){
+__global__ __launch_bounds__(256) void k_decide(const float* __restrict__ nc, float* __restrict__ ws){
   int t = threadIdx.x;
   Scal* sc = (Scal*)(ws + OFF_SCAL);
-  float stepf = (float)step_p[0];
-  float egb = eg_b[0];
-  int gid = blockIdx.x*256 + t;
-  int gstride = gridDim.x*256;
-  unsigned long long bm = 0ULL, bs = 0ULL;
-  for (int s = gid; s < S_N; s += gstride){
-    float a = out[OUT_AT + s];
-    float x = (stepf - a) / 1000.0f;
-    float lp = 0.0f;
-    #pragma unroll
-    for (int j=0;j<32;j++) lp += fmaxf(x*el_w[j] + el_b[j], 0.0f) * eg_w[j];
-    float er = sigmoidf_(lp + ws[OFF_CONF + s] + egb);
-    float sa = stepf - a;
-    bool recent = (a >= 0.0f) && (sa < 3.0f);
-    float msk = recent ? 0.0f : er;
-    ws[OFF_ERSC + s] = er;
-    ws[OFF_MASKED + s] = msk;
-    ws[OFF_SLOTAGE + s] = sa;
-    unsigned long long pm = packvi(msk, s); if (pm > bm) bm = pm;
-    unsigned long long ps = packvi(sa,  s); if (ps > bs) bs = ps;
-  }
-  __shared__ unsigned long long rm[256], rs[256];
-  rm[t]=bm; rs[t]=bs; __syncthreads();
-  for (int o=128;o>0;o>>=1){
-    if (t<o){ if (rm[t+o]>rm[t]) rm[t]=rm[t+o]; if (rs[t+o]>rs[t]) rs[t]=rs[t+o]; }
-    __syncthreads();
-  }
+  __shared__ int stip[192], sap[192], seff[192];
+  __shared__ float red[64];
+  if (t < 192){ stip[t] = ((int*)(ws+OFF_TI))[t]; sap[t] = ((int*)(ws+OFF_APPLY))[t]; }
+  if (t < 64) red[t] = ws[OFF_STORES + t];
+  __syncthreads();
+  if (t < 32) red[t] += red[t+32];
+  __syncthreads();
+  if (t < 16) red[t] += red[t+16];
+  __syncthreads();
+  if (t < 8)  red[t] += red[t+8];
+  __syncthreads();
   if (t == 0){
-    atomicMax(&sc->masked_pack, rm[0]);
-    atomicMax(&sc->slotage_pack, rs[0]);
-  }
-}
-
-__global__ __launch_bounds__(64) void k_decide(const float* __restrict__ nc, float* __restrict__ ws){
-  int t = threadIdx.x;
-  Scal* sc = (Scal*)(ws + OFF_SCAL);
-  __shared__ float red[64];
-  red[t] = ws[OFF_STORES + t];
-  __syncthreads();
-  for (int o=32;o>0;o>>=1){ if (t<o) red[t]+=red[t+o]; __syncthreads(); }
-  if (t == 0){
-    float store_mean = red[0] / 64.0f;
+    float store_mean = (red[0]+red[1]+red[2]+red[3]+red[4]+red[5]+red[6]+red[7]) / 64.0f;
     int cnt = sc->cnt_active;
     float capacity = (float)cnt / 65536.0f;
     float dyn_thr;
@@ -584,8 +607,7 @@
     int base_store = store_mean > raw_thr;
     int novelty_ok = sc->nov_mean > dyn_thr;
     int cmax = cnt > 1 ? cnt : 1;
-    float denom = (float)(64 * cmax);
-    float perc = (cnt > 0) ? ((float)sc->cond_cnt) / denom : 1.0f;
+    float perc = (cnt > 0) ? ((float)sc->cond_cnt) / (float)(64 * cmax) : 1.0f;
     int topk_ok = perc > topk_thr;
     int de = sc->do_erase;
     int ss = base_store && novelty_ok && topk_ok;
@@ -596,40 +618,62 @@
     sc->should_store = ss;
     sc->write_idx = de ? sc->victim_idx : ((mmax > 0.0f) ? marg : sarg);
   }
-  __syncthreads();
-  const int* ap = (const int*)(ws + OFF_APPLY);
-  for (int d=t; d<512; d+=64){
+  if (t < 192){
+    int k = t % 3, b = t / 3, row = stip[t];
+    int bmax = -1;
+    for (int bp=0;bp<64;bp++) if (stip[bp*3+k] == row) bmax = bp;
+    seff[t] = (b == bmax && sap[t]) ? 1 : 0;
+  }
+  __syncthreads();
+  if (t < 192){
+    int k = t % 3, row = stip[t];
+    int winv = seff[t];
+    if (winv){
+      for (int pp=0;pp<192;pp++)
+        if (seff[pp] && stip[pp] == row && (pp % 3) > k){ winv = 0; break; }
+    }
+    ((int*)(ws+OFF_WIN))[t] = winv;
+  }
+  __syncthreads();
+  for (int d=t; d<512; d+=256){
     float v = nc[d];
-    if (ap[0]) v = ws[OFF_DNC0 + 0*512 + d];
-    if (ap[1]) v = ws[OFF_DNC0 + 1*512 + d];
-    if (ap[2]) v = ws[OFF_DNC0 + 2*512 + d];
+    if (sap[0]) v = ws[OFF_DNC0 + 0*512 + d];
+    if (sap[1]) v = ws[OFF_DNC0 + 1*512 + d];
+    if (sap[2]) v = ws[OFF_DNC0 + 2*512 + d];
     ws[OFF_DRIFT0 + d] = v;
   }
 }
 
-__global__ __launch_bounds__(256) void k_finalout(const int* __restrict__ step_p,
-                                                  float* __restrict__ ws, float* __restrict__ out){
+__global__ __launch_bounds__(256) void k_final(const int* __restrict__ step_p,
+                                               float* __restrict__ ws, float* __restrict__ out){
   int blk = blockIdx.x, t = threadIdx.x;
   Scal* sc = (Scal*)(ws + OFF_SCAL);
   int ss = sc->should_store, de = sc->do_erase;
-  if (blk == 64){
-    if (ss){
-      int wi = sc->write_idx;
-      for (int d=t; d<512; d+=256) out[OUT_MEM + (size_t)wi*512 + d] = ws[OFF_DRIFT0 + d];
-      if (t == 0){
-        out[OUT_AT + wi] = (float)step_p[0];
-        touch_row(wi, ws);
-      }
-    }
-    return;
-  }
-  float mmax = mono2f((unsigned)(sc->masked_pack >> 32));
-  bool usemask = ss && !de;
-  for (int s = blk*256 + t; s < S_N; s += 64*256){
-    float v;
-    if (usemask) v = (mmax <= 0.0f) ? ws[OFF_SLOTAGE + s] : ws[OFF_MASKED + s];
-    else v = ws[OFF_ERSC + s];
-    out[OUT_ER + s] = v;
+  if (blk < 64){
+    float mmax = mono2f((unsigned)(sc->masked_pack >> 32));
+    bool usemask = ss && !de;
+    for (int s = blk*1024 + t; s < (blk+1)*1024; s += 256){
+      float v;
+      if (usemask) v = (mmax <= 0.0f) ? ws[OFF_SLOTAGE + s] : ws[OFF_MASKED + s];
+      else v = ws[OFF_ERSC + s];
+      out[OUT_ER + s] = v;
+    }
+  } else if (blk < 256){
+    int p = blk - 64;
+    if (!((const int*)(ws+OFF_WIN))[p]) return;
+    int row = ((const int*)(ws+OFF_TI))[p];
+    if (ss && row == sc->write_idx) return;
+    if (t == 0) touch_row(row, ws);
+    for (int d=t; d<512; d+=256)
+      out[OUT_MEM + (size_t)row*512 + d] = ws[OFF_DOCAND + p*512 + d];
+  } else {
+    if (!ss) return;
+    int wi = sc->write_idx;
+    for (int d=t; d<512; d+=256) out[OUT_MEM + (size_t)wi*512 + d] = ws[OFF_DRIFT0 + d];
+    if (t == 0){
+      out[OUT_AT + wi] = (float)step_p[0];
+      touch_row(wi, ws);
+    }
   }
 }
 
@@ -650,13 +694,14 @@
   __shared__ float red[256];
   red[t] = lsum; __syncthreads();
   for (int o=128;o>0;o>>=1){ if (t<o) red[t]+=red[t+o]; __syncthreads(); }
-  if (t == 0 && red[0] != 0.0f) atomicAdd(&sc->changed_sum, red[0]);
-}
-
-__global__ void k_rc(float* __restrict__ ws, float* __restrict__ out){
-  if (threadIdx.x == 0 && blockIdx.x == 0){
-    Scal* sc = (Scal*)(ws + OFF_SCAL);
-    out[OUT_RC] = sc->changed_sum / 33554432.0f;
+  if (t == 0){
+    if (red[0] != 0.0f) atomicAdd(&sc->changed_sum, red[0]);
+    __threadfence();
+    int d = atomicAdd(&sc->done, 1);
+    if (d == (int)gridDim.x - 1){
+      float cs = atomicAdd(&sc->changed_sum, 0.0f);
+      out[OUT_RC] = cs / 33554432.0f;
+    }
   }
 }
 
@@ -695,21 +740,15 @@
   float* out = (float*)d_out;
   float* ws  = (float*)d_ws;
 
-  k_init     <<<dim3(289), dim3(256), 0, stream>>>(nc, at, ec_w, step, ws, out);
-  k_mlp1a    <<<dim3(128), dim3(256), 0, stream>>>(nc, qr, sr_w1, ws);
-  k_phase1   <<<dim3(1024), dim3(256), 0, stream>>>(mem, ec_b, eg_w, ws, out);
-  k_mlp1b    <<<dim3(65), dim3(256), 0, stream>>>(nc, qr, sr_b1, sr_g, sr_be,
-                                                  sr_w2, sr_b2, sn_w, sn_b, sg_w, sg_b, ws, out);
-  k_scan     <<<dim3(512), dim3(256), 0, stream>>>(at, step, ws);
-  k_victimfix<<<dim3(1), dim3(256), 0, stream>>>(ec_b, eg_w, ws, out);
-  k_top3     <<<dim3(64), dim3(256), 0, stream>>>(ws);
-  k_mlp2     <<<dim3(256), dim3(256), 0, stream>>>(nc, dd_w1, ds_w1, ws, out);
-  k_pairfin  <<<dim3(192), dim3(256), 0, stream>>>(nc, dd_b1, dd_w2, dd_b2,
-                                                   ds_b1, ds_w2, ds_b2, ws, out);
-  k_scatter  <<<dim3(8), dim3(64), 0, stream>>>(ws, out);
-  k_erase    <<<dim3(64), dim3(256), 0, stream>>>(step, el_w, el_b, eg_w, eg_b, ws, out);
-  k_decide   <<<dim3(1), dim3(64), 0, stream>>>(nc, ws);
-  k_finalout <<<dim3(65), dim3(256), 0, stream>>>(step, ws, out);
-  k_diff     <<<dim3(64), dim3(256), 0, stream>>>(mem, ws, out);
-  k_rc       <<<dim3(1), dim3(64), 0, stream>>>(ws, out);
-}
+  k_init   <<<dim3(353),  dim3(256), 0, stream>>>(nc, qr, at, ec_w, step,
+                sr_w1, sr_b1, sr_g, sr_be, sr_w2, sr_b2, sn_w, sn_b, sg_w, sg_b, ws, out);
+  k_phase1 <<<dim3(1024), dim3(256), 0, stream>>>(mem, ec_b, eg_w, ws, out);
+  k_scan   <<<dim3(832),  dim3(256), 0, stream>>>(at, step, el_w, el_b, eg_w, eg_b, ws, out);
+  k_victop <<<dim3(129),  dim3(256), 0, stream>>>(step, el_w, el_b, eg_w, eg_b, ec_b, ws, out);
+  k_mlp2   <<<dim3(256),  dim3(256), 0, stream>>>(nc, dd_w1, ds_w1, ws, out);
+  k_pairfin<<<dim3(192),  dim3(256), 0, stream>>>(nc, dd_b1, dd_w2, dd_b2,
+                                                  ds_b1, ds_w2, ds_b2, ws, out);
+  k_decide <<<dim3(1),    dim3(256), 0, stream>>>(nc, ws);
+  k_final  <<<dim3(257),  dim3(256), 0, stream>>>(step, ws, out);
+  k_diff   <<<dim3(64),   dim3(256), 0, stream>>>(mem, ws, out);
+}
```
